# Optimization experiments

Measured on AMD Instinct MI355X. Metric: run time of the kernel, lower is better.

## Reference

```python
import jax, jax.numpy as jnp
import numpy as np

ALPHA = 0.2  # LeakyReLU negative slope
NEG_INF = -9e15  # matches torch -9000000000000000.0


def setup_inputs() -> dict:
    key = jax.random.key(0)
    k1, k2, k3, k4, k5, k6 = jax.random.split(key, 6)
    N, F_in, F_out = 4096, 512, 256
    adj = jax.random.randint(k1, (N, N), 0, 2, dtype=jnp.int32)
    h = jax.random.normal(k2, (N, F_in), dtype=jnp.float32)
    # proj: Linear(F_in, F_out)
    W = jax.random.normal(k3, (F_in, F_out), dtype=jnp.float32) * (1.0 / np.sqrt(F_in))
    b = jax.random.normal(k4, (F_out,), dtype=jnp.float32) * 0.01
    # proj_a: Linear(2*F_out, 1) split into the two halves acting on src/dst features
    a1 = jax.random.normal(k5, (F_out,), dtype=jnp.float32) * (1.0 / np.sqrt(2 * F_out))
    a2 = jax.random.normal(k6, (F_out,), dtype=jnp.float32) * (1.0 / np.sqrt(2 * F_out))
    a_b = jnp.zeros((), dtype=jnp.float32)
    return {"adj": adj, "h": h, "W": W, "b": b, "a1": a1, "a2": a2, "a_b": a_b}


def reference(adj, h, W, b, a1, a2, a_b):
    # wh = proj(h): [N, F_out]
    wh = h @ W + b
    # Fused form of the N x N x 2F concat + Linear(2F,1):
    # logits[i, j] = wh[i] . a1 + wh[j] . a2 + a_b
    f_src = wh @ a1  # [N]
    f_dst = wh @ a2  # [N]
    e = jax.nn.leaky_relu(f_src[:, None] + f_dst[None, :] + a_b, negative_slope=ALPHA)
    e = jnp.where(adj > 0, e, NEG_INF)
    att = jax.nn.softmax(e, axis=-1)  # F.softmax legacy dim=1 for 2D
    # dropout: inference mode (no-op) for deterministic reference
    out = att @ wh  # [N, F_out]
    return jax.nn.elu(out)  # concat=True
```

## Files before the change

kernel.cpp:

```cpp
#include <hip/hip_runtime.h>

#define NN   4096
#define FIN  512
#define FOUT 256
#define ALPHA 0.2f

typedef __attribute__((ext_vector_type(8))) short short8;
typedef __attribute__((ext_vector_type(4))) float f32x4;
typedef unsigned short u16;

__device__ __forceinline__ u16 f2bf(float x) {
    union { float f; unsigned u; } v; v.f = x;
    unsigned r = v.u + 0x7FFF + ((v.u >> 16) & 1);
    return (u16)(r >> 16);
}

__global__ __launch_bounds__(256) void k_wt(const float* __restrict__ W,
                                            u16* __restrict__ Wt) {
    __shared__ float s[64 * 65];
    const int t  = threadIdx.x;
    const int f0 = blockIdx.x * 64;
    const int k0 = blockIdx.y * 64;
    #pragma unroll
    for (int p = 0; p < 4; ++p) {
        int q = t + 256 * p, rr = q >> 4, cc = q & 15;
        float4 w4 = *(const float4*)&W[(size_t)(k0 + rr) * FOUT + f0 + cc * 4];
        s[(cc * 4 + 0) * 65 + rr] = w4.x;
        s[(cc * 4 + 1) * 65 + rr] = w4.y;
        s[(cc * 4 + 2) * 65 + rr] = w4.z;
        s[(cc * 4 + 3) * 65 + rr] = w4.w;
    }
    __syncthreads();
    #pragma unroll
    for (int p = 0; p < 4; ++p) {
        int q = t + 256 * p, f = q >> 4, kg = q & 15;
        ushort4 o;
        o.x = f2bf(s[f * 65 + kg * 4 + 0]);
        o.y = f2bf(s[f * 65 + kg * 4 + 1]);
        o.z = f2bf(s[f * 65 + kg * 4 + 2]);
        o.w = f2bf(s[f * 65 + kg * 4 + 3]);
        *(ushort4*)&Wt[(size_t)(f0 + f) * FIN + k0 + kg * 4] = o;
    }
}

#define HS 520
__global__ __launch_bounds__(256) void k_proj(const float* __restrict__ h,
                                              const u16* __restrict__ Wt,
                                              const float* __restrict__ bias,
                                              float* __restrict__ wh,
                                              u16* __restrict__ whT) {
    __shared__ u16 s_h[32 * HS];
    const int t  = threadIdx.x;
    const int f0 = blockIdx.x * 64;
    const int i0 = blockIdx.y * 32;
    #pragma unroll
    for (int p = 0; p < 16; ++p) {
        int q = t + 256 * p, row = q >> 7, c4 = q & 127;
        float4 v = *(const float4*)&h[(size_t)(i0 + row) * FIN + c4 * 4];
        ushort4 o; o.x = f2bf(v.x); o.y = f2bf(v.y); o.z = f2bf(v.z); o.w = f2bf(v.w);
        *(ushort4*)&s_h[row * HS + c4 * 4] = o;
    }
    __syncthreads();
    const int w = t >> 6, l = t & 63, n = l & 15, quad = l >> 4;
    const int hh = w & 1, fh = w >> 1;
    f32x4 acc[2] = {{0.f,0.f,0.f,0.f},{0.f,0.f,0.f,0.f}};
    #pragma unroll
    for (int k0 = 0; k0 < FIN; k0 += 32) {
        short8 a = *(const short8*)&s_h[(hh * 16 + n) * HS + k0 + quad * 8];
        short8 b0 = *(const short8*)&Wt[(size_t)(f0 + fh * 32 + n) * FIN + k0 + quad * 8];
        short8 b1 = *(const short8*)&Wt[(size_t)(f0 + fh * 32 + 16 + n) * FIN + k0 + quad * 8];
        acc[0] = __builtin_amdgcn_mfma_f32_16x16x32_bf16(a, b0, acc[0], 0, 0, 0);
        acc[1] = __builtin_amdgcn_mfma_f32_16x16x32_bf16(a, b1, acc[1], 0, 0, 0);
    }
    u16* wt_tile = whT + (size_t)(i0 >> 5) * (FOUT * 32);
    #pragma unroll
    for (int u = 0; u < 2; ++u) {
        const int f = f0 + fh * 32 + u * 16 + n;
        const float bv = bias[f];
        #pragma unroll
        for (int r = 0; r < 4; ++r) {
            const int i = i0 + hh * 16 + quad * 4 + r;
            float val = acc[u][r] + bv;
            wh[(size_t)i * FOUT + f] = val;
            wt_tile[f * 32 + (i - i0)] = f2bf(val);
        }
    }
}

__global__ __launch_bounds__(256) void k_vec(const float* __restrict__ wh,
                                             const float* __restrict__ a1,
                                             const float* __restrict__ a2,
                                             const float* __restrict__ ab,
                                             float* __restrict__ fs,
                                             float* __restrict__ fd) {
    const int i = blockIdx.x * 4 + (threadIdx.x >> 6);
    const int t = threadIdx.x & 63;
    float4 w  = ((const float4*)(wh + (size_t)i * FOUT))[t];
    float4 v1 = ((const float4*)a1)[t];
    float4 v2 = ((const float4*)a2)[t];
    float d1 = w.x*v1.x + w.y*v1.y + w.z*v1.z + w.w*v1.w;
    float d2 = w.x*v2.x + w.y*v2.y + w.z*v2.z + w.w*v2.w;
    #pragma unroll
    for (int off = 32; off > 0; off >>= 1) {
        d1 += __shfl_down(d1, off);
        d2 += __shfl_down(d2, off);
    }
    if (t == 0) { fs[i] = d1 + ab[0]; fd[i] = d2; }
}

#define BI 32
#define TJ 64
#define PS 72
__global__ __launch_bounds__(256) void k_attn(const int* __restrict__ adj,
                                              const u16* __restrict__ whT,
                                              const float* __restrict__ fs,
                                              const float* __restrict__ fd,
                                              float* __restrict__ part,
                                              float* __restrict__ psum) {
    __shared__ u16 s_p[BI * PS];
    const int t  = threadIdx.x;
    const int i0 = blockIdx.x * BI;
    const int c  = blockIdx.y;
    const int jchunk = NN / gridDim.y;
    const int jbeg = c * jchunk, jend = jbeg + jchunk;
    const int jq = t & 15, rh = t >> 4;
    const float fs0 = fs[i0 + rh], fs1 = fs[i0 + rh + 16];
    const int w = t >> 6, l = t & 63, n = l & 15, quad = l >> 4;

    f32x4 acc[2][4] = {{{0.f,0.f,0.f,0.f},{0.f,0.f,0.f,0.f},{0.f,0.f,0.f,0.f},{0.f,0.f,0.f,0.f}},
                       {{0.f,0.f,0.f,0.f},{0.f,0.f,0.f,0.f},{0.f,0.f,0.f,0.f},{0.f,0.f,0.f,0.f}}};
    float rs0 = 0.f, rs1 = 0.f;

    int4   av0 = *(const int4*)&adj[(size_t)(i0 + rh) * NN + jbeg + jq * 4];
    int4   av1 = *(const int4*)&adj[(size_t)(i0 + rh + 16) * NN + jbeg + jq * 4];
    float4 fdv = *(const float4*)&fd[jbeg + jq * 4];

    for (int j0 = jbeg; j0 < jend; j0 += TJ) {
        ushort4 o0, o1;
        {
            float x, p;
            x = fs0 + fdv.x; x = x > 0.f ? x : ALPHA * x; p = av0.x > 0 ? __expf(x) : 0.f; o0.x = f2bf(p); rs0 += p;
            x = fs0 + fdv.y; x = x > 0.f ? x : ALPHA * x; p = av0.y > 0 ? __expf(x) : 0.f; o0.y = f2bf(p); rs0 += p;
            x = fs0 + fdv.z; x = x > 0.f ? x : ALPHA * x; p = av0.z > 0 ? __expf(x) : 0.f; o0.z = f2bf(p); rs0 += p;
            x = fs0 + fdv.w; x = x > 0.f ? x : ALPHA * x; p = av0.w > 0 ? __expf(x) : 0.f; o0.w = f2bf(p); rs0 += p;
            x = fs1 + fdv.x; x = x > 0.f ? x : ALPHA * x; p = av1.x > 0 ? __expf(x) : 0.f; o1.x = f2bf(p); rs1 += p;
            x = fs1 + fdv.y; x = x > 0.f ? x : ALPHA * x; p = av1.y > 0 ? __expf(x) : 0.f; o1.y = f2bf(p); rs1 += p;
            x = fs1 + fdv.z; x = x > 0.f ? x : ALPHA * x; p = av1.z > 0 ? __expf(x) : 0.f; o1.z = f2bf(p); rs1 += p;
            x = fs1 + fdv.w; x = x > 0.f ? x : ALPHA * x; p = av1.w > 0 ? __expf(x) : 0.f; o1.w = f2bf(p); rs1 += p;
        }
        __syncthreads();
        *(ushort4*)&s_p[rh * PS + jq * 4]        = o0;
        *(ushort4*)&s_p[(rh + 16) * PS + jq * 4] = o1;
        if (j0 + TJ < jend) {
            av0 = *(const int4*)&adj[(size_t)(i0 + rh) * NN + j0 + TJ + jq * 4];
            av1 = *(const int4*)&adj[(size_t)(i0 + rh + 16) * NN + j0 + TJ + jq * 4];
            fdv = *(const float4*)&fd[j0 + TJ + jq * 4];
        }
        short8 b[2][4];
        #pragma unroll
        for (int s = 0; s < 2; ++s) {
            const u16* tb = whT + (size_t)((j0 >> 5) + s) * (FOUT * 32) + quad * 8;
            #pragma unroll
            for (int u = 0; u < 4; ++u)
                b[s][u] = *(const short8*)&tb[(w * 64 + u * 16 + n) * 32];
        }
        __syncthreads();
        #pragma unroll
        for (int s = 0; s < 2; ++s) {
            short8 a0 = *(const short8*)&s_p[n * PS + s * 32 + quad * 8];
            short8 a1f = *(const short8*)&s_p[(16 + n) * PS + s * 32 + quad * 8];
            #pragma unroll
            for (int u = 0; u < 4; ++u) {
                acc[0][u] = __builtin_amdgcn_mfma_f32_16x16x32_bf16(a0,  b[s][u], acc[0][u], 0, 0, 0);
                acc[1][u] = __builtin_amdgcn_mfma_f32_16x16x32_bf16(a1f, b[s][u], acc[1][u], 0, 0, 0);
            }
        }
    }
    #pragma unroll
    for (int m = 8; m > 0; m >>= 1) {
        rs0 += __shfl_xor(rs0, m);
        rs1 += __shfl_xor(rs1, m);
    }
    if (jq == 0) {
        psum[(size_t)c * NN + i0 + rh]      = rs0;
        psum[(size_t)c * NN + i0 + rh + 16] = rs1;
    }
    float* pc = part + ((size_t)c * NN + i0) * FOUT;
    #pragma unroll
    for (int hf = 0; hf < 2; ++hf)
        #pragma unroll
        for (int u = 0; u < 4; ++u)
            #pragma unroll
            for (int r = 0; r < 4; ++r)
                pc[(size_t)(hf * 16 + quad * 4 + r) * FOUT + w * 64 + u * 16 + n] = acc[hf][u][r];
}

__global__ __launch_bounds__(256) void k_fin(const float* __restrict__ part,
                                             const float* __restrict__ psum,
                                             float* __restrict__ out, int C) {
    const int g = blockIdx.x * 256 + threadIdx.x;
    const int i = g >> 6;
    const size_t s4 = (size_t)NN * FOUT / 4;
    float4 a = ((const float4*)part)[g];
    float s = psum[i];
    for (int c = 1; c < C; ++c) {
        float4 bb = ((const float4*)part)[g + (size_t)c * s4];
        a.x += bb.x; a.y += bb.y; a.z += bb.z; a.w += bb.w;
        s += psum[(size_t)c * NN + i];
    }
    const float inv = 1.0f / s;
    a.x *= inv; a.y *= inv; a.z *= inv; a.w *= inv;
    a.x = a.x > 0.f ? a.x : __expf(a.x) - 1.f;
    a.y = a.y > 0.f ? a.y : __expf(a.y) - 1.f;
    a.z = a.z > 0.f ? a.z : __expf(a.z) - 1.f;
    a.w = a.w > 0.f ? a.w : __expf(a.w) - 1.f;
    ((float4*)out)[g] = a;
}

extern "C" void kernel_launch(void* const* d_in, const int* in_sizes, int n_in,
                              void* d_out, int out_size, void* d_ws, size_t ws_size,
                              hipStream_t stream) {
    const int*   adj = (const int*)  d_in[0];
    const float* h   = (const float*)d_in[1];
    const float* W   = (const float*)d_in[2];
    const float* b   = (const float*)d_in[3];
    const float* a1  = (const float*)d_in[4];
    const float* a2  = (const float*)d_in[5];
    const float* ab  = (const float*)d_in[6];
    float* out = (float*)d_out;

    auto need = [](int c) -> size_t {
        size_t fl = (size_t)NN * FOUT + 2 * NN + (size_t)c * NN + (size_t)c * NN * FOUT;
        size_t us = (size_t)FOUT * FIN + (size_t)NN * FOUT;
        return fl * 4 + us * 2;
    };
    int C = 4;
    while (C > 1 && need(C) > ws_size) C >>= 1;

    float* wh   = (float*)d_ws;
    float* fs   = wh + (size_t)NN * FOUT;
    float* fd   = fs + NN;
    float* psum = fd + NN;
    float* part = psum + (size_t)C * NN;
    u16*   Wt   = (u16*)(part + (size_t)C * NN * FOUT);
    u16*   whT  = Wt + (size_t)FOUT * FIN;

    k_wt  <<<dim3(FOUT / 64, FIN / 64), 256, 0, stream>>>(W, Wt);
    k_proj<<<dim3(FOUT / 64, NN / 32), 256, 0, stream>>>(h, Wt, b, wh, whT);
    k_vec <<<NN / 4, 256, 0, stream>>>(wh, a1, a2, ab, fs, fd);
    k_attn<<<dim3(NN / BI, C), 256, 0, stream>>>(adj, whT, fs, fd, part, psum);
    k_fin <<<(NN * FOUT / 4) / 256, 256, 0, stream>>>(part, psum, out, C);
}
```

Measured before the change: 151.2 us.

## Fuse attention-vector dot products into projection and double-buffer attention P tiles

Removes the separate k_vec kernel and the fp32 wh buffer. The projection epilogue now computes partial dot products with a1/a2, reduces them across lanes with shuffles, and accumulates them into fs/fd with atomics. fs/fd are zeroed inside k_wt, and a_b is added later in k_attn. The attention kernel now double-buffers the shared P tile with an XOR swizzle, which drops one barrier per iteration, issues the whT loads earlier, and raises wave priority around the MFMAs. Atomic accumulation makes fs/fd summation order nondeterministic.

After: 149.7 us. About the same (-1.0%).

```diff
diff --git a/kernel.cpp b/kernel.cpp
--- a/kernel.cpp
+++ b/kernel.cpp
@@ -16,9 +16,13 @@
 }
 
 __global__ __launch_bounds__(256) void k_wt(const float* __restrict__ W,
-                                            u16* __restrict__ Wt) {
+                                            u16* __restrict__ Wt,
+                                            float* __restrict__ fs,
+                                            float* __restrict__ fd) {
     __shared__ float s[64 * 65];
     const int t  = threadIdx.x;
+    const int g  = (blockIdx.y * gridDim.x + blockIdx.x) * 256 + t;
+    if (g < NN) fs[g] = 0.f; else fd[g - NN] = 0.f;
     const int f0 = blockIdx.x * 64;
     const int k0 = blockIdx.y * 64;
     #pragma unroll
@@ -47,8 +51,11 @@
 __global__ __launch_bounds__(256) void k_proj(const float* __restrict__ h,
                                               const u16* __restrict__ Wt,
                                               const float* __restrict__ bias,
-                                              float* __restrict__ wh,
-                                              u16* __restrict__ whT) {
+                                              const float* __restrict__ a1,
+                                              const float* __restrict__ a2,
+                                              u16* __restrict__ whT,
+                                              float* __restrict__ fs,
+                                              float* __restrict__ fd) {
     __shared__ u16 s_h[32 * HS];
     const int t  = threadIdx.x;
     const int f0 = blockIdx.x * 64;
@@ -72,59 +79,58 @@
         acc[0] = __builtin_amdgcn_mfma_f32_16x16x32_bf16(a, b0, acc[0], 0, 0, 0);
         acc[1] = __builtin_amdgcn_mfma_f32_16x16x32_bf16(a, b1, acc[1], 0, 0, 0);
     }
+    const int fb = f0 + fh * 32 + n;
+    const float bv0 = bias[fb],  bv1 = bias[fb + 16];
+    const float a10 = a1[fb],    a11 = a1[fb + 16];
+    const float a20 = a2[fb],    a21 = a2[fb + 16];
     u16* wt_tile = whT + (size_t)(i0 >> 5) * (FOUT * 32);
-    #pragma unroll
-    for (int u = 0; u < 2; ++u) {
-        const int f = f0 + fh * 32 + u * 16 + n;
-        const float bv = bias[f];
+    float d1[4], d2[4];
+    #pragma unroll
+    for (int r = 0; r < 4; ++r) {
+        const int ic = hh * 16 + quad * 4 + r;
+        const float v0 = acc[0][r] + bv0;
+        const float v1 = acc[1][r] + bv1;
+        wt_tile[fb * 32 + ic]        = f2bf(v0);
+        wt_tile[(fb + 16) * 32 + ic] = f2bf(v1);
+        d1[r] = v0 * a10 + v1 * a11;
+        d2[r] = v0 * a20 + v1 * a21;
+    }
+    #pragma unroll
+    for (int m = 1; m < 16; m <<= 1) {
+        #pragma unroll
+        for (int r = 0; r < 4; ++r) {
+            d1[r] += __shfl_xor(d1[r], m);
+            d2[r] += __shfl_xor(d2[r], m);
+        }
+    }
+    if (n == 0) {
         #pragma unroll
         for (int r = 0; r < 4; ++r) {
             const int i = i0 + hh * 16 + quad * 4 + r;
-            float val = acc[u][r] + bv;
-            wh[(size_t)i * FOUT + f] = val;
-            wt_tile[f * 32 + (i - i0)] = f2bf(val);
-        }
-    }
-}
-
-__global__ __launch_bounds__(256) void k_vec(const float* __restrict__ wh,
-                                             const float* __restrict__ a1,
-                                             const float* __restrict__ a2,
-                                             const float* __restrict__ ab,
-                                             float* __restrict__ fs,
-                                             float* __restrict__ fd) {
-    const int i = blockIdx.x * 4 + (threadIdx.x >> 6);
-    const int t = threadIdx.x & 63;
-    float4 w  = ((const float4*)(wh + (size_t)i * FOUT))[t];
-    float4 v1 = ((const float4*)a1)[t];
-    float4 v2 = ((const float4*)a2)[t];
-    float d1 = w.x*v1.x + w.y*v1.y + w.z*v1.z + w.w*v1.w;
-    float d2 = w.x*v2.x + w.y*v2.y + w.z*v2.z + w.w*v2.w;
-    #pragma unroll
-    for (int off = 32; off > 0; off >>= 1) {
-        d1 += __shfl_down(d1, off);
-        d2 += __shfl_down(d2, off);
-    }
-    if (t == 0) { fs[i] = d1 + ab[0]; fd[i] = d2; }
+            atomicAdd(&fs[i], d1[r]);
+            atomicAdd(&fd[i], d2[r]);
+        }
+    }
 }
 
 #define BI 32
 #define TJ 64
-#define PS 72
 __global__ __launch_bounds__(256) void k_attn(const int* __restrict__ adj,
                                               const u16* __restrict__ whT,
                                               const float* __restrict__ fs,
                                               const float* __restrict__ fd,
+                                              const float* __restrict__ ab,
                                               float* __restrict__ part,
                                               float* __restrict__ psum) {
-    __shared__ u16 s_p[BI * PS];
+    __shared__ u16 s_p[2][BI * 64];
     const int t  = threadIdx.x;
     const int i0 = blockIdx.x * BI;
     const int c  = blockIdx.y;
     const int jchunk = NN / gridDim.y;
     const int jbeg = c * jchunk, jend = jbeg + jchunk;
     const int jq = t & 15, rh = t >> 4;
-    const float fs0 = fs[i0 + rh], fs1 = fs[i0 + rh + 16];
+    const float fs0 = fs[i0 + rh] + ab[0];
+    const float fs1 = fs[i0 + rh + 16] + ab[0];
     const int w = t >> 6, l = t & 63, n = l & 15, quad = l >> 4;
 
     f32x4 acc[2][4] = {{{0.f,0.f,0.f,0.f},{0.f,0.f,0.f,0.f},{0.f,0.f,0.f,0.f},{0.f,0.f,0.f,0.f}},
@@ -135,7 +141,18 @@
     int4   av1 = *(const int4*)&adj[(size_t)(i0 + rh + 16) * NN + jbeg + jq * 4];
     float4 fdv = *(const float4*)&fd[jbeg + jq * 4];
 
+    const int wbase = rh * 128 + ((jq * 8) ^ ((rh & 7) << 4));
+    const int rsw   = (n & 7) << 4;
+    int pb = 0;
     for (int j0 = jbeg; j0 < jend; j0 += TJ) {
+        short8 b[2][4];
+        #pragma unroll
+        for (int s = 0; s < 2; ++s) {
+            const u16* tb = whT + (size_t)((j0 >> 5) + s) * (FOUT * 32) + quad * 8;
+            #pragma unroll
+            for (int u = 0; u < 4; ++u)
+                b[s][u] = *(const short8*)&tb[(w * 64 + u * 16 + n) * 32];
+        }
         ushort4 o0, o1;
         {
             float x, p;
@@ -148,33 +165,29 @@
             x = fs1 + fdv.z; x = x > 0.f ? x : ALPHA * x; p = av1.z > 0 ? __expf(x) : 0.f; o1.z = f2bf(p); rs1 += p;
             x = fs1 + fdv.w; x = x > 0.f ? x : ALPHA * x; p = av1.w > 0 ? __expf(x) : 0.f; o1.w = f2bf(p); rs1 += p;
         }
-        __syncthreads();
-        *(ushort4*)&s_p[rh * PS + jq * 4]        = o0;
-        *(ushort4*)&s_p[(rh + 16) * PS + jq * 4] = o1;
+        char* spB = (char*)s_p + pb * 4096;
+        *(ushort4*)(spB + wbase)        = o0;
+        *(ushort4*)(spB + 2048 + wbase) = o1;
         if (j0 + TJ < jend) {
             av0 = *(const int4*)&adj[(size_t)(i0 + rh) * NN + j0 + TJ + jq * 4];
             av1 = *(const int4*)&adj[(size_t)(i0 + rh + 16) * NN + j0 + TJ + jq * 4];
             fdv = *(const float4*)&fd[j0 + TJ + jq * 4];
         }
-        short8 b[2][4];
+        __syncthreads();
+        __builtin_amdgcn_s_setprio(1);
         #pragma unroll
         for (int s = 0; s < 2; ++s) {
-            const u16* tb = whT + (size_t)((j0 >> 5) + s) * (FOUT * 32) + quad * 8;
-            #pragma unroll
-            for (int u = 0; u < 4; ++u)
-                b[s][u] = *(const short8*)&tb[(w * 64 + u * 16 + n) * 32];
-        }
-        __syncthreads();
-        #pragma unroll
-        for (int s = 0; s < 2; ++s) {
-            short8 a0 = *(const short8*)&s_p[n * PS + s * 32 + quad * 8];
-            short8 a1f = *(const short8*)&s_p[(16 + n) * PS + s * 32 + quad * 8];
+            const int rb = n * 128 + ((s * 64 + quad * 16) ^ rsw);
+            short8 a0  = *(const short8*)(spB + rb);
+            short8 a1f = *(const short8*)(spB + 2048 + rb);
             #pragma unroll
             for (int u = 0; u < 4; ++u) {
                 acc[0][u] = __builtin_amdgcn_mfma_f32_16x16x32_bf16(a0,  b[s][u], acc[0][u], 0, 0, 0);
                 acc[1][u] = __builtin_amdgcn_mfma_f32_16x16x32_bf16(a1f, b[s][u], acc[1][u], 0, 0, 0);
             }
         }
+        __builtin_amdgcn_s_setprio(0);
+        pb ^= 1;
     }
     #pragma unroll
     for (int m = 8; m > 0; m >>= 1) {
@@ -230,24 +243,22 @@
     float* out = (float*)d_out;
 
     auto need = [](int c) -> size_t {
-        size_t fl = (size_t)NN * FOUT + 2 * NN + (size_t)c * NN + (size_t)c * NN * FOUT;
+        size_t fl = 2 * NN + (size_t)c * NN + (size_t)c * NN * FOUT;
         size_t us = (size_t)FOUT * FIN + (size_t)NN * FOUT;
         return fl * 4 + us * 2;
     };
     int C = 4;
     while (C > 1 && need(C) > ws_size) C >>= 1;
 
-    float* wh   = (float*)d_ws;
-    float* fs   = wh + (size_t)NN * FOUT;
+    float* fs   = (float*)d_ws;
     float* fd   = fs + NN;
     float* psum = fd + NN;
     float* part = psum + (size_t)C * NN;
     u16*   Wt   = (u16*)(part + (size_t)C * NN * FOUT);
     u16*   whT  = Wt + (size_t)FOUT * FIN;
 
-    k_wt  <<<dim3(FOUT / 64, FIN / 64), 256, 0, stream>>>(W, Wt);
-    k_proj<<<dim3(FOUT / 64, NN / 32), 256, 0, stream>>>(h, Wt, b, wh, whT);
-    k_vec <<<NN / 4, 256, 0, stream>>>(wh, a1, a2, ab, fs, fd);
-    k_attn<<<dim3(NN / BI, C), 256, 0, stream>>>(adj, whT, fs, fd, part, psum);
+    k_wt  <<<dim3(FOUT / 64, FIN / 64), 256, 0, stream>>>(W, Wt, fs, fd);
+    k_proj<<<dim3(FOUT / 64, NN / 32), 256, 0, stream>>>(h, Wt, b, a1, a2, whT, fs, fd);
+    k_attn<<<dim3(NN / BI, C), 256, 0, stream>>>(adj, whT, fs, fd, ab, part, psum);
     k_fin <<<(NN * FOUT / 4) / 256, 256, 0, stream>>>(part, psum, out, C);
 }
```
